# Performance work log

Measured on AMD Instinct MI355X. Metric: run time of the kernel, lower is better.

## Reference

```python
import jax, jax.numpy as jnp
import numpy as np

LN_EPS = 1e-5


def setup_inputs() -> dict:
    key = jax.random.key(0)
    ks = jax.random.split(key, 10)
    N, E, B = 20000, 320000, 16
    node_dim, cond_dim, out_dim = 256, 512, 256
    return {
        "node_feats": jax.random.normal(ks[0], (N, node_dim), dtype=jnp.float32),
        "cond_feats": jax.random.normal(ks[1], (B, cond_dim), dtype=jnp.float32),
        "batch_ids": jax.random.randint(ks[2], (N,), 0, B),
        "node_j_ids": jax.random.randint(ks[3], (E,), 0, N),
        "node_i_ids": jax.random.randint(ks[4], (E,), 0, N),
        "edge_w": jax.random.uniform(ks[5], (E, 1), dtype=jnp.float32),
        "edge_p": jax.random.uniform(ks[6], (E, 1), dtype=jnp.float32),
        "Wc": jax.random.normal(ks[7], (cond_dim, 2 * out_dim), dtype=jnp.float32) * (cond_dim ** -0.5),
        "bc": jax.random.normal(ks[8], (2 * out_dim,), dtype=jnp.float32) * 0.02,
        "Wl": jax.random.normal(ks[9], (node_dim, out_dim), dtype=jnp.float32) * (node_dim ** -0.5),
    }


def reference(node_feats, cond_feats, batch_ids, node_j_ids, node_i_ids,
              edge_w, edge_p, Wc, bc, Wl):
    N = node_feats.shape[0]
    # --- FiLM fusion ---
    gb = cond_feats @ Wc + bc                       # [B, 2*out_dim]
    gamma, beta = jnp.split(gb, 2, axis=-1)
    gamma = gamma + 1.0
    x = node_feats @ Wl                             # [N, out_dim]
    # non-affine LayerNorm over last dim
    mu = jnp.mean(x, axis=-1, keepdims=True)
    var = jnp.mean(jnp.square(x - mu), axis=-1, keepdims=True)
    x = (x - mu) * jax.lax.rsqrt(var + LN_EPS)
    x = x * gamma[batch_ids] + beta[batch_ids]      # per-node FiLM via batch gather
    x = jax.nn.relu(x)
    # --- message passing: gather -> weight -> scatter-add ---
    edge_weights = edge_w * edge_p                  # [E, 1]
    msg = x[node_j_ids] * edge_weights              # [E, out_dim]
    agg = jax.ops.segment_sum(msg, node_i_ids, num_segments=N)
    return jax.nn.relu(agg)
```

## Files before the change

### kernel.cpp

```cpp
#include <hip/hip_runtime.h>
#include <hip/hip_bf16.h>

#define OUT_DIM 256
#define COND_DIM 512
#define NODE_DIM 256
#define TM 32
#define LDA 264
#define LN_EPS 1e-5f
#define CAP 64
#define POISON 0xAAAAAAAAu
#define CHUNK 4096
#define EPT 16
#define NBINS 256
#define BCAP 2560

typedef __attribute__((ext_vector_type(8))) short bf16x8;
typedef __attribute__((ext_vector_type(8))) unsigned short u16x8;
typedef __attribute__((ext_vector_type(4))) float f32x4;

__device__ inline unsigned short f2bf(float f) {
    unsigned u = __float_as_uint(f);
    u += 0x7fffu + ((u >> 16) & 1u);
    return (unsigned short)(u >> 16);
}
__device__ inline float bf2f(unsigned short b) {
    return __uint_as_float((unsigned)b << 16);
}

__global__ __launch_bounds__(256) void f1_prep_kernel(
        const int* __restrict__ ni, const int* __restrict__ nj,
        const float* __restrict__ ew, const float* __restrict__ ep,
        unsigned* __restrict__ gcur, unsigned* __restrict__ coarse_ij,
        float* __restrict__ coarse_w, int E, int f1b,
        const float* __restrict__ Wl, unsigned short* __restrict__ WlT,
        const float* __restrict__ cond, const float* __restrict__ Wc,
        const float* __restrict__ bc, float* __restrict__ gamma, float* __restrict__ beta) {
    __shared__ float lds[64 * 65];
    __shared__ unsigned cnt[NBINS], base[NBINS];
    int t = threadIdx.x;

    if (blockIdx.x < (unsigned)f1b) {
        cnt[t] = 0;
        __syncthreads();
        unsigned ijr[EPT]; float wr[EPT]; unsigned rbr[EPT];
        int e0 = blockIdx.x * CHUNK;
        #pragma unroll
        for (int k = 0; k < EPT; ++k) {
            int e = e0 + k * 256 + t;
            if (e < E) {
                unsigned i = (unsigned)ni[e];
                unsigned j = (unsigned)nj[e];
                float w = ew[e] * ep[e];
                unsigned b = i >> 7;
                unsigned r = atomicAdd(&cnt[b], 1u);
                ijr[k] = (i << 16) | j;
                wr[k]  = w;
                rbr[k] = r | (b << 20);
            } else rbr[k] = 0xFFFFFFFFu;
        }
        __syncthreads();
        {
            unsigned c = cnt[t];
            base[t] = c ? (atomicAdd(&gcur[t], c) - POISON) : 0u;
        }
        __syncthreads();
        #pragma unroll
        for (int k = 0; k < EPT; ++k) {
            if (rbr[k] != 0xFFFFFFFFu) {
                unsigned b = rbr[k] >> 20;
                unsigned pos = base[b] + (rbr[k] & 0xFFFFFu);
                if (pos < BCAP) {
                    unsigned idx = b * BCAP + pos;
                    coarse_ij[idx] = ijr[k];
                    coarse_w[idx]  = wr[k];
                }
            }
        }
        return;
    }

    int pb = blockIdx.x - f1b;
    if (pb < 16) {
        float (*tile)[65] = (float(*)[65])lds;
        int bx = pb & 3, by = pb >> 2;
        int tr = t >> 6, tc = t & 63;
        #pragma unroll
        for (int rr = 0; rr < 64; rr += 4)
            tile[rr + tr][tc] = Wl[(by * 64 + rr + tr) * OUT_DIM + bx * 64 + tc];
        __syncthreads();
        #pragma unroll
        for (int rr = 0; rr < 64; rr += 4) {
            int n = bx * 64 + rr + tr;
            int k = by * 64 + tc;
            WlT[n * NODE_DIM + k] = f2bf(tile[tc][rr + tr]);
        }
    } else {
        int bf = pb - 16;
        int b = bf >> 1, half = bf & 1;
        int o = half * 256 + t;
        float* c = lds;
        for (int k = t; k < COND_DIM; k += 256) c[k] = cond[b * COND_DIM + k];
        __syncthreads();
        float acc = bc[o];
        for (int k = 0; k < COND_DIM; k += 4) {
            float4 cv = *(const float4*)&c[k];
            acc += cv.x * Wc[(k + 0) * 512 + o];
            acc += cv.y * Wc[(k + 1) * 512 + o];
            acc += cv.z * Wc[(k + 2) * 512 + o];
            acc += cv.w * Wc[(k + 3) * 512 + o];
        }
        if (half == 0) gamma[b * 256 + t] = acc + 1.0f;
        else           beta[b * 256 + t] = acc;
    }
}

__global__ __launch_bounds__(256) void f2_gemm_kernel(
        const unsigned* __restrict__ gcur, const unsigned* __restrict__ coarse_ij,
        const float* __restrict__ coarse_w, unsigned* __restrict__ epk,
        unsigned* __restrict__ cursor, int NB,
        const float* __restrict__ nf, const unsigned short* __restrict__ WlT,
        const int* __restrict__ batch_ids, const float* __restrict__ gamma,
        const float* __restrict__ beta, unsigned short* __restrict__ xout, int N) {
    __shared__ __align__(16) unsigned short Atile[TM * LDA];
    __shared__ float part_s[TM][2], part_s2[TM][2];
    __shared__ int bid_s[TM];
    __shared__ unsigned lcur[128];
    int t = threadIdx.x;

    if (blockIdx.x < (unsigned)NB) {
        int b = blockIdx.x;
        if (t < 128) lcur[t] = 0;
        __syncthreads();
        unsigned cntb = gcur[b] - POISON;
        if (cntb > BCAP) cntb = BCAP;
        for (unsigned r = t; r < cntb; r += 256) {
            unsigned ij = coarse_ij[(unsigned)b * BCAP + r];
            float w = coarse_w[(unsigned)b * BCAP + r];
            unsigned i = ij >> 16;
            unsigned c = atomicAdd(&lcur[i & 127u], 1u);
            if (c < CAP)
                epk[(i << 6) + c] = (ij & 0xFFFFu) | ((unsigned)f2bf(w) << 16);
        }
        __syncthreads();
        if (t < 128) cursor[(unsigned)b * 128 + t] = lcur[t];
        return;
    }

    int n0 = (blockIdx.x - NB) * TM;

    #pragma unroll
    for (int it = 0; it < 8; ++it) {
        int idx = t + it * 256;
        int r = idx >> 6;
        int c4 = idx & 63;
        int row = n0 + r;
        float4 v;
        if (row < N) v = *(const float4*)&nf[(size_t)row * NODE_DIM + c4 * 4];
        else         v = make_float4(0.f, 0.f, 0.f, 0.f);
        unsigned* dst = (unsigned*)&Atile[r * LDA + c4 * 4];
        dst[0] = (unsigned)f2bf(v.x) | ((unsigned)f2bf(v.y) << 16);
        dst[1] = (unsigned)f2bf(v.z) | ((unsigned)f2bf(v.w) << 16);
    }
    if (t < TM) bid_s[t] = (n0 + t < N) ? batch_ids[n0 + t] : 0;
    __syncthreads();

    int wave = t >> 6;
    int lane = t & 63;
    int l = lane & 15;
    int quad = lane >> 4;
    int rowbase = (wave & 1) * 16;
    int colbase = (wave >> 1) * 128;
    int half = wave >> 1;

    f32x4 acc[8];
    #pragma unroll
    for (int ct = 0; ct < 8; ++ct) acc[ct] = (f32x4){0.f, 0.f, 0.f, 0.f};

    const unsigned short* Abase = &Atile[(rowbase + l) * LDA + quad * 8];
    const unsigned short* Bbase = &WlT[(colbase + l) * NODE_DIM + quad * 8];

    #pragma unroll
    for (int ks = 0; ks < 8; ++ks) {
        bf16x8 a = *(const bf16x8*)(Abase + ks * 32);
        #pragma unroll
        for (int ct = 0; ct < 8; ++ct) {
            bf16x8 b = *(const bf16x8*)(Bbase + ct * 16 * NODE_DIM + ks * 32);
            acc[ct] = __builtin_amdgcn_mfma_f32_16x16x32_bf16(a, b, acc[ct], 0, 0, 0);
        }
    }

    #pragma unroll
    for (int reg = 0; reg < 4; ++reg) {
        float s = 0.f, s2 = 0.f;
        #pragma unroll
        for (int ct = 0; ct < 8; ++ct) {
            float v = acc[ct][reg];
            s += v; s2 += v * v;
        }
        #pragma unroll
        for (int off = 1; off <= 8; off <<= 1) {
            s += __shfl_xor(s, off);
            s2 += __shfl_xor(s2, off);
        }
        if (l == 0) {
            int r = rowbase + quad * 4 + reg;
            part_s[r][half] = s;
            part_s2[r][half] = s2;
        }
    }
    __syncthreads();

    #pragma unroll
    for (int reg = 0; reg < 4; ++reg) {
        int lrow = rowbase + quad * 4 + reg;
        float S = part_s[lrow][0] + part_s[lrow][1];
        float S2 = part_s2[lrow][0] + part_s2[lrow][1];
        float mu = S * (1.f / OUT_DIM);
        float var = S2 * (1.f / OUT_DIM) - mu * mu;
        float rs = rsqrtf(var + LN_EPS);
        int grow = n0 + lrow;
        int bid = bid_s[lrow];
        const float* gg = &gamma[bid * OUT_DIM];
        const float* gb = &beta[bid * OUT_DIM];
        if (grow < N) {
            unsigned short* orow = &xout[(size_t)grow * OUT_DIM];
            #pragma unroll
            for (int ct = 0; ct < 8; ++ct) {
                int col = colbase + ct * 16 + l;
                float v = (acc[ct][reg] - mu) * rs;
                v = v * gg[col] + gb[col];
                orow[col] = f2bf(fmaxf(v, 0.f));
            }
        }
    }
}

__global__ void agg_kernel(const unsigned short* __restrict__ x, const unsigned* __restrict__ epk,
                           const unsigned* __restrict__ cursor, float* __restrict__ out, int N) {
    int node = blockIdx.x * 4 + (threadIdx.x >> 6);
    int lane = threadIdx.x & 63;
    if (node >= N) return;
    int deg = (int)cursor[node];
    if (deg > CAP) deg = CAP;
    int s = node << 6;
    int e = s + deg;
    int half = lane >> 5;
    int li = lane & 31;

    float a[8];
    #pragma unroll
    for (int k = 0; k < 8; ++k) a[k] = 0.f;

    {
        unsigned pk[8];
        #pragma unroll
        for (int q = 0; q < 8; ++q) pk[q] = epk[s + 2 * q + half];
        float w[8];
        #pragma unroll
        for (int q = 0; q < 8; ++q)
            w[q] = (2 * q + half < deg) ? bf2f((unsigned short)(pk[q] >> 16)) : 0.f;
        u16x8 v[8];
        #pragma unroll
        for (int q = 0; q < 8; ++q)
            v[q] = *(const u16x8*)&x[(size_t)(pk[q] & 0xFFFFu) * OUT_DIM + li * 8];
        #pragma unroll
        for (int q = 0; q < 8; ++q) {
            #pragma unroll
            for (int k = 0; k < 8; ++k) a[k] += bf2f(v[q][k]) * w[q];
        }
    }

    for (int p = s + 16; p < e; p += 8) {
        int i0 = p + 0 + half, i1 = p + 2 + half, i2 = p + 4 + half, i3 = p + 6 + half;
        unsigned pk0 = epk[i0];
        unsigned pk1 = epk[i1];
        unsigned pk2 = epk[i2];
        unsigned pk3 = epk[i3];
        u16x8 v0 = *(const u16x8*)&x[(size_t)(pk0 & 0xFFFFu) * OUT_DIM + li * 8];
        u16x8 v1 = *(const u16x8*)&x[(size_t)(pk1 & 0xFFFFu) * OUT_DIM + li * 8];
        u16x8 v2 = *(const u16x8*)&x[(size_t)(pk2 & 0xFFFFu) * OUT_DIM + li * 8];
        u16x8 v3 = *(const u16x8*)&x[(size_t)(pk3 & 0xFFFFu) * OUT_DIM + li * 8];
        float w0 = (i0 < e) ? bf2f((unsigned short)(pk0 >> 16)) : 0.f;
        float w1 = (i1 < e) ? bf2f((unsigned short)(pk1 >> 16)) : 0.f;
        float w2 = (i2 < e) ? bf2f((unsigned short)(pk2 >> 16)) : 0.f;
        float w3 = (i3 < e) ? bf2f((unsigned short)(pk3 >> 16)) : 0.f;
        #pragma unroll
        for (int k = 0; k < 8; ++k) {
            a[k] += bf2f(v0[k]) * w0;
            a[k] += bf2f(v1[k]) * w1;
            a[k] += bf2f(v2[k]) * w2;
            a[k] += bf2f(v3[k]) * w3;
        }
    }

    #pragma unroll
    for (int k = 0; k < 8; ++k) a[k] += __shfl_xor(a[k], 32);

    f32x4 o;
    int kb = half * 4;
    o[0] = fmaxf(a[kb + 0], 0.f);
    o[1] = fmaxf(a[kb + 1], 0.f);
    o[2] = fmaxf(a[kb + 2], 0.f);
    o[3] = fmaxf(a[kb + 3], 0.f);
    __builtin_nontemporal_store(o, (f32x4*)&out[(size_t)node * OUT_DIM + li * 8 + kb]);
}

extern "C" void kernel_launch(void* const* d_in, const int* in_sizes, int n_in,
                              void* d_out, int out_size, void* d_ws, size_t ws_size,
                              hipStream_t stream) {
    const float* node_feats = (const float*)d_in[0];
    const float* cond_feats = (const float*)d_in[1];
    const int*   batch_ids  = (const int*)d_in[2];
    const int*   node_j     = (const int*)d_in[3];
    const int*   node_i     = (const int*)d_in[4];
    const float* edge_w     = (const float*)d_in[5];
    const float* edge_p     = (const float*)d_in[6];
    const float* Wc         = (const float*)d_in[7];
    const float* bc         = (const float*)d_in[8];
    const float* Wl         = (const float*)d_in[9];
    float* out = (float*)d_out;

    const int N = in_sizes[2];
    const int E = in_sizes[3];
    const int B = in_sizes[1] / COND_DIM;

    const int NB = (N + 127) / 128;

    char* ws = (char*)d_ws;
    float* gamma     = (float*)ws;  ws += (size_t)B * OUT_DIM * 4;
    float* beta      = (float*)ws;  ws += (size_t)B * OUT_DIM * 4;
    unsigned short* x   = (unsigned short*)ws;  ws += (size_t)N * OUT_DIM * 2;
    unsigned short* WlT = (unsigned short*)ws;  ws += (size_t)NODE_DIM * OUT_DIM * 2;
    unsigned* cursor = (unsigned*)ws;  ws += (size_t)NB * 128 * 4;
    unsigned* epk    = (unsigned*)ws;  ws += (size_t)N * CAP * 4;
    unsigned* gcur   = (unsigned*)ws;  ws += (size_t)NBINS * 4;
    unsigned* coarse_ij = (unsigned*)ws;  ws += (size_t)NBINS * BCAP * 4;
    float*    coarse_w  = (float*)ws;     ws += (size_t)NBINS * BCAP * 4;

    int nblk = (N + TM - 1) / TM;
    int f1b = (E + CHUNK - 1) / CHUNK;

    f1_prep_kernel<<<f1b + 48, 256, 0, stream>>>(node_i, node_j, edge_w, edge_p,
                                                 gcur, coarse_ij, coarse_w, E, f1b,
                                                 Wl, WlT, cond_feats, Wc, bc, gamma, beta);
    f2_gemm_kernel<<<NB + nblk, 256, 0, stream>>>(gcur, coarse_ij, coarse_w, epk, cursor, NB,
                                                  node_feats, WlT, batch_ids,
                                                  gamma, beta, x, N);
    agg_kernel<<<(N + 3) / 4, 256, 0, stream>>>(x, epk, cursor, out, N);
}
```

Before: 153.2 us.

## Fuse three kernels into one cooperative persistent kernel with grid syncs

Merges the prep, bin/GEMM and aggregation kernels into a single cooperative kernel that loops over work units in a persistent grid, separating phases with grid.sync(). The goal is to remove the launch gaps and tail effects between three kernel launches. In exchange, grid-wide barriers cost something, occupancy is capped by the cooperative grid (at most 1024 blocks under launch_bounds(256,4)), and the phases that used to run as large grids now run as strided loops. Grid size is cached in a static variable after the first call.

Result: slower. 327.5 us (+113.7%).

```diff
diff --git a/kernel.cpp b/kernel.cpp
--- a/kernel.cpp
+++ b/kernel.cpp
@@ -1,5 +1,8 @@
 #include <hip/hip_runtime.h>
+#include <hip/hip_cooperative_groups.h>
 #include <hip/hip_bf16.h>
+
+namespace cg = cooperative_groups;
 
 #define OUT_DIM 256
 #define COND_DIM 512
@@ -27,282 +30,281 @@
     return __uint_as_float((unsigned)b << 16);
 }
 
-__global__ __launch_bounds__(256) void f1_prep_kernel(
+__global__ __launch_bounds__(256, 4) void fused_kernel(
         const int* __restrict__ ni, const int* __restrict__ nj,
         const float* __restrict__ ew, const float* __restrict__ ep,
-        unsigned* __restrict__ gcur, unsigned* __restrict__ coarse_ij,
-        float* __restrict__ coarse_w, int E, int f1b,
-        const float* __restrict__ Wl, unsigned short* __restrict__ WlT,
-        const float* __restrict__ cond, const float* __restrict__ Wc,
-        const float* __restrict__ bc, float* __restrict__ gamma, float* __restrict__ beta) {
-    __shared__ float lds[64 * 65];
-    __shared__ unsigned cnt[NBINS], base[NBINS];
+        const float* __restrict__ Wl, const float* __restrict__ cond,
+        const float* __restrict__ Wc, const float* __restrict__ bc,
+        const float* __restrict__ nf, const int* __restrict__ batch_ids,
+        unsigned short* __restrict__ WlT, float* __restrict__ gamma, float* __restrict__ beta,
+        unsigned* __restrict__ gcur, unsigned* __restrict__ coarse_ij, float* __restrict__ coarse_w,
+        unsigned* __restrict__ epk, unsigned* __restrict__ cursor,
+        unsigned short* __restrict__ x, float* __restrict__ out,
+        int E, int N, int f1b, int NB, int nblk) {
+    cg::grid_group grid = cg::this_grid();
     int t = threadIdx.x;
 
-    if (blockIdx.x < (unsigned)f1b) {
-        cnt[t] = 0;
-        __syncthreads();
-        unsigned ijr[EPT]; float wr[EPT]; unsigned rbr[EPT];
-        int e0 = blockIdx.x * CHUNK;
-        #pragma unroll
-        for (int k = 0; k < EPT; ++k) {
-            int e = e0 + k * 256 + t;
-            if (e < E) {
-                unsigned i = (unsigned)ni[e];
-                unsigned j = (unsigned)nj[e];
-                float w = ew[e] * ep[e];
-                unsigned b = i >> 7;
-                unsigned r = atomicAdd(&cnt[b], 1u);
-                ijr[k] = (i << 16) | j;
-                wr[k]  = w;
-                rbr[k] = r | (b << 20);
-            } else rbr[k] = 0xFFFFFFFFu;
-        }
-        __syncthreads();
-        {
-            unsigned c = cnt[t];
-            base[t] = c ? (atomicAdd(&gcur[t], c) - POISON) : 0u;
-        }
-        __syncthreads();
-        #pragma unroll
-        for (int k = 0; k < EPT; ++k) {
-            if (rbr[k] != 0xFFFFFFFFu) {
-                unsigned b = rbr[k] >> 20;
-                unsigned pos = base[b] + (rbr[k] & 0xFFFFFu);
-                if (pos < BCAP) {
-                    unsigned idx = b * BCAP + pos;
-                    coarse_ij[idx] = ijr[k];
-                    coarse_w[idx]  = wr[k];
-                }
-            }
-        }
-        return;
-    }
-
-    int pb = blockIdx.x - f1b;
-    if (pb < 16) {
-        float (*tile)[65] = (float(*)[65])lds;
-        int bx = pb & 3, by = pb >> 2;
-        int tr = t >> 6, tc = t & 63;
-        #pragma unroll
-        for (int rr = 0; rr < 64; rr += 4)
-            tile[rr + tr][tc] = Wl[(by * 64 + rr + tr) * OUT_DIM + bx * 64 + tc];
-        __syncthreads();
-        #pragma unroll
-        for (int rr = 0; rr < 64; rr += 4) {
-            int n = bx * 64 + rr + tr;
-            int k = by * 64 + tc;
-            WlT[n * NODE_DIM + k] = f2bf(tile[tc][rr + tr]);
-        }
-    } else {
-        int bf = pb - 16;
-        int b = bf >> 1, half = bf & 1;
-        int o = half * 256 + t;
-        float* c = lds;
-        for (int k = t; k < COND_DIM; k += 256) c[k] = cond[b * COND_DIM + k];
-        __syncthreads();
-        float acc = bc[o];
-        for (int k = 0; k < COND_DIM; k += 4) {
-            float4 cv = *(const float4*)&c[k];
-            acc += cv.x * Wc[(k + 0) * 512 + o];
-            acc += cv.y * Wc[(k + 1) * 512 + o];
-            acc += cv.z * Wc[(k + 2) * 512 + o];
-            acc += cv.w * Wc[(k + 3) * 512 + o];
-        }
-        if (half == 0) gamma[b * 256 + t] = acc + 1.0f;
-        else           beta[b * 256 + t] = acc;
-    }
-}
-
-__global__ __launch_bounds__(256) void f2_gemm_kernel(
-        const unsigned* __restrict__ gcur, const unsigned* __restrict__ coarse_ij,
-        const float* __restrict__ coarse_w, unsigned* __restrict__ epk,
-        unsigned* __restrict__ cursor, int NB,
-        const float* __restrict__ nf, const unsigned short* __restrict__ WlT,
-        const int* __restrict__ batch_ids, const float* __restrict__ gamma,
-        const float* __restrict__ beta, unsigned short* __restrict__ xout, int N) {
     __shared__ __align__(16) unsigned short Atile[TM * LDA];
     __shared__ float part_s[TM][2], part_s2[TM][2];
     __shared__ int bid_s[TM];
     __shared__ unsigned lcur[128];
-    int t = threadIdx.x;
-
-    if (blockIdx.x < (unsigned)NB) {
-        int b = blockIdx.x;
-        if (t < 128) lcur[t] = 0;
+    __shared__ unsigned cnt[NBINS], base[NBINS];
+
+    for (int u = blockIdx.x; u < f1b + 48; u += gridDim.x) {
         __syncthreads();
-        unsigned cntb = gcur[b] - POISON;
-        if (cntb > BCAP) cntb = BCAP;
-        for (unsigned r = t; r < cntb; r += 256) {
-            unsigned ij = coarse_ij[(unsigned)b * BCAP + r];
-            float w = coarse_w[(unsigned)b * BCAP + r];
-            unsigned i = ij >> 16;
-            unsigned c = atomicAdd(&lcur[i & 127u], 1u);
-            if (c < CAP)
-                epk[(i << 6) + c] = (ij & 0xFFFFu) | ((unsigned)f2bf(w) << 16);
-        }
-        __syncthreads();
-        if (t < 128) cursor[(unsigned)b * 128 + t] = lcur[t];
-        return;
-    }
-
-    int n0 = (blockIdx.x - NB) * TM;
-
-    #pragma unroll
-    for (int it = 0; it < 8; ++it) {
-        int idx = t + it * 256;
-        int r = idx >> 6;
-        int c4 = idx & 63;
-        int row = n0 + r;
-        float4 v;
-        if (row < N) v = *(const float4*)&nf[(size_t)row * NODE_DIM + c4 * 4];
-        else         v = make_float4(0.f, 0.f, 0.f, 0.f);
-        unsigned* dst = (unsigned*)&Atile[r * LDA + c4 * 4];
-        dst[0] = (unsigned)f2bf(v.x) | ((unsigned)f2bf(v.y) << 16);
-        dst[1] = (unsigned)f2bf(v.z) | ((unsigned)f2bf(v.w) << 16);
-    }
-    if (t < TM) bid_s[t] = (n0 + t < N) ? batch_ids[n0 + t] : 0;
-    __syncthreads();
-
-    int wave = t >> 6;
-    int lane = t & 63;
-    int l = lane & 15;
-    int quad = lane >> 4;
-    int rowbase = (wave & 1) * 16;
-    int colbase = (wave >> 1) * 128;
-    int half = wave >> 1;
-
-    f32x4 acc[8];
-    #pragma unroll
-    for (int ct = 0; ct < 8; ++ct) acc[ct] = (f32x4){0.f, 0.f, 0.f, 0.f};
-
-    const unsigned short* Abase = &Atile[(rowbase + l) * LDA + quad * 8];
-    const unsigned short* Bbase = &WlT[(colbase + l) * NODE_DIM + quad * 8];
-
-    #pragma unroll
-    for (int ks = 0; ks < 8; ++ks) {
-        bf16x8 a = *(const bf16x8*)(Abase + ks * 32);
-        #pragma unroll
-        for (int ct = 0; ct < 8; ++ct) {
-            bf16x8 b = *(const bf16x8*)(Bbase + ct * 16 * NODE_DIM + ks * 32);
-            acc[ct] = __builtin_amdgcn_mfma_f32_16x16x32_bf16(a, b, acc[ct], 0, 0, 0);
+        if (u < f1b) {
+            cnt[t] = 0;
+            __syncthreads();
+            unsigned ijr[EPT]; float wr[EPT]; unsigned rbr[EPT];
+            int e0 = u * CHUNK;
+            #pragma unroll
+            for (int k = 0; k < EPT; ++k) {
+                int e = e0 + k * 256 + t;
+                if (e < E) {
+                    unsigned i = (unsigned)ni[e];
+                    unsigned j = (unsigned)nj[e];
+                    float w = ew[e] * ep[e];
+                    unsigned b = i >> 7;
+                    unsigned r = atomicAdd(&cnt[b], 1u);
+                    ijr[k] = (i << 16) | j;
+                    wr[k]  = w;
+                    rbr[k] = r | (b << 20);
+                } else rbr[k] = 0xFFFFFFFFu;
+            }
+            __syncthreads();
+            {
+                unsigned c = cnt[t];
+                base[t] = c ? (atomicAdd(&gcur[t], c) - POISON) : 0u;
+            }
+            __syncthreads();
+            #pragma unroll
+            for (int k = 0; k < EPT; ++k) {
+                if (rbr[k] != 0xFFFFFFFFu) {
+                    unsigned b = rbr[k] >> 20;
+                    unsigned pos = base[b] + (rbr[k] & 0xFFFFFu);
+                    if (pos < BCAP) {
+                        unsigned idx = b * BCAP + pos;
+                        coarse_ij[idx] = ijr[k];
+                        coarse_w[idx]  = wr[k];
+                    }
+                }
+            }
+        } else {
+            int pb = u - f1b;
+            if (pb < 16) {
+                float (*tile)[65] = (float(*)[65])Atile;
+                int bx = pb & 3, by = pb >> 2;
+                int tr = t >> 6, tc = t & 63;
+                #pragma unroll
+                for (int rr = 0; rr < 64; rr += 4)
+                    tile[rr + tr][tc] = Wl[(by * 64 + rr + tr) * OUT_DIM + bx * 64 + tc];
+                __syncthreads();
+                #pragma unroll
+                for (int rr = 0; rr < 64; rr += 4) {
+                    int n = bx * 64 + rr + tr;
+                    int k = by * 64 + tc;
+                    WlT[n * NODE_DIM + k] = f2bf(tile[tc][rr + tr]);
+                }
+            } else {
+                int bf = pb - 16;
+                int b = bf >> 1, half = bf & 1;
+                int o = half * 256 + t;
+                float* c = (float*)Atile;
+                for (int k = t; k < COND_DIM; k += 256) c[k] = cond[b * COND_DIM + k];
+                __syncthreads();
+                float acc = bc[o];
+                for (int k = 0; k < COND_DIM; k += 4) {
+                    float4 cv = *(const float4*)&c[k];
+                    acc += cv.x * Wc[(k + 0) * 512 + o];
+                    acc += cv.y * Wc[(k + 1) * 512 + o];
+                    acc += cv.z * Wc[(k + 2) * 512 + o];
+                    acc += cv.w * Wc[(k + 3) * 512 + o];
+                }
+                if (half == 0) gamma[b * 256 + t] = acc + 1.0f;
+                else           beta[b * 256 + t] = acc;
+            }
         }
     }
-
-    #pragma unroll
-    for (int reg = 0; reg < 4; ++reg) {
-        float s = 0.f, s2 = 0.f;
-        #pragma unroll
-        for (int ct = 0; ct < 8; ++ct) {
-            float v = acc[ct][reg];
-            s += v; s2 += v * v;
-        }
-        #pragma unroll
-        for (int off = 1; off <= 8; off <<= 1) {
-            s += __shfl_xor(s, off);
-            s2 += __shfl_xor(s2, off);
-        }
-        if (l == 0) {
-            int r = rowbase + quad * 4 + reg;
-            part_s[r][half] = s;
-            part_s2[r][half] = s2;
+    grid.sync();
+
+    for (int u = blockIdx.x; u < NB + nblk; u += gridDim.x) {
+        __syncthreads();
+        if (u < NB) {
+            int b = u;
+            if (t < 128) lcur[t] = 0;
+            __syncthreads();
+            unsigned cntb = gcur[b] - POISON;
+            if (cntb > BCAP) cntb = BCAP;
+            for (unsigned r = t; r < cntb; r += 256) {
+                unsigned ij = coarse_ij[(unsigned)b * BCAP + r];
+                float w = coarse_w[(unsigned)b * BCAP + r];
+                unsigned i = ij >> 16;
+                unsigned c = atomicAdd(&lcur[i & 127u], 1u);
+                if (c < CAP)
+                    epk[(i << 6) + c] = (ij & 0xFFFFu) | ((unsigned)f2bf(w) << 16);
+            }
+            __syncthreads();
+            if (t < 128) cursor[(unsigned)b * 128 + t] = lcur[t];
+        } else {
+            int n0 = (u - NB) * TM;
+            #pragma unroll
+            for (int it = 0; it < 8; ++it) {
+                int idx = t + it * 256;
+                int r = idx >> 6;
+                int c4 = idx & 63;
+                int row = n0 + r;
+                float4 v;
+                if (row < N) v = *(const float4*)&nf[(size_t)row * NODE_DIM + c4 * 4];
+                else         v = make_float4(0.f, 0.f, 0.f, 0.f);
+                unsigned* dst = (unsigned*)&Atile[r * LDA + c4 * 4];
+                dst[0] = (unsigned)f2bf(v.x) | ((unsigned)f2bf(v.y) << 16);
+                dst[1] = (unsigned)f2bf(v.z) | ((unsigned)f2bf(v.w) << 16);
+            }
+            if (t < TM) bid_s[t] = (n0 + t < N) ? batch_ids[n0 + t] : 0;
+            __syncthreads();
+
+            int wave = t >> 6;
+            int lane = t & 63;
+            int l = lane & 15;
+            int quad = lane >> 4;
+            int rowbase = (wave & 1) * 16;
+            int colbase = (wave >> 1) * 128;
+            int half = wave >> 1;
+
+            f32x4 acc[8];
+            #pragma unroll
+            for (int ct = 0; ct < 8; ++ct) acc[ct] = (f32x4){0.f, 0.f, 0.f, 0.f};
+
+            const unsigned short* Abase = &Atile[(rowbase + l) * LDA + quad * 8];
+            const unsigned short* Bbase = &WlT[(colbase + l) * NODE_DIM + quad * 8];
+
+            #pragma unroll
+            for (int ks = 0; ks < 8; ++ks) {
+                bf16x8 a = *(const bf16x8*)(Abase + ks * 32);
+                #pragma unroll
+                for (int ct = 0; ct < 8; ++ct) {
+                    bf16x8 b = *(const bf16x8*)(Bbase + ct * 16 * NODE_DIM + ks * 32);
+                    acc[ct] = __builtin_amdgcn_mfma_f32_16x16x32_bf16(a, b, acc[ct], 0, 0, 0);
+                }
+            }
+
+            #pragma unroll
+            for (int reg = 0; reg < 4; ++reg) {
+                float s = 0.f, s2 = 0.f;
+                #pragma unroll
+                for (int ct = 0; ct < 8; ++ct) {
+                    float v = acc[ct][reg];
+                    s += v; s2 += v * v;
+                }
+                #pragma unroll
+                for (int off = 1; off <= 8; off <<= 1) {
+                    s += __shfl_xor(s, off);
+                    s2 += __shfl_xor(s2, off);
+                }
+                if (l == 0) {
+                    int r = rowbase + quad * 4 + reg;
+                    part_s[r][half] = s;
+                    part_s2[r][half] = s2;
+                }
+            }
+            __syncthreads();
+
+            #pragma unroll
+            for (int reg = 0; reg < 4; ++reg) {
+                int lrow = rowbase + quad * 4 + reg;
+                float S = part_s[lrow][0] + part_s[lrow][1];
+                float S2 = part_s2[lrow][0] + part_s2[lrow][1];
+                float mu = S * (1.f / OUT_DIM);
+                float var = S2 * (1.f / OUT_DIM) - mu * mu;
+                float rs = rsqrtf(var + LN_EPS);
+                int grow = n0 + lrow;
+                int bid = bid_s[lrow];
+                const float* gg = &gamma[bid * OUT_DIM];
+                const float* gb = &beta[bid * OUT_DIM];
+                if (grow < N) {
+                    unsigned short* orow = &x[(size_t)grow * OUT_DIM];
+                    #pragma unroll
+                    for (int ct = 0; ct < 8; ++ct) {
+                        int col = colbase + ct * 16 + l;
+                        float v = (acc[ct][reg] - mu) * rs;
+                        v = v * gg[col] + gb[col];
+                        orow[col] = f2bf(fmaxf(v, 0.f));
+                    }
+                }
+            }
         }
     }
-    __syncthreads();
-
-    #pragma unroll
-    for (int reg = 0; reg < 4; ++reg) {
-        int lrow = rowbase + quad * 4 + reg;
-        float S = part_s[lrow][0] + part_s[lrow][1];
-        float S2 = part_s2[lrow][0] + part_s2[lrow][1];
-        float mu = S * (1.f / OUT_DIM);
-        float var = S2 * (1.f / OUT_DIM) - mu * mu;
-        float rs = rsqrtf(var + LN_EPS);
-        int grow = n0 + lrow;
-        int bid = bid_s[lrow];
-        const float* gg = &gamma[bid * OUT_DIM];
-        const float* gb = &beta[bid * OUT_DIM];
-        if (grow < N) {
-            unsigned short* orow = &xout[(size_t)grow * OUT_DIM];
-            #pragma unroll
-            for (int ct = 0; ct < 8; ++ct) {
-                int col = colbase + ct * 16 + l;
-                float v = (acc[ct][reg] - mu) * rs;
-                v = v * gg[col] + gb[col];
-                orow[col] = f2bf(fmaxf(v, 0.f));
+    grid.sync();
+
+    int ngroups = (N + 3) >> 2;
+    for (int g = blockIdx.x; g < ngroups; g += gridDim.x) {
+        int node = g * 4 + (t >> 6);
+        if (node >= N) continue;
+        int lane = t & 63;
+        int deg = (int)cursor[node];
+        if (deg > CAP) deg = CAP;
+        int s = node << 6;
+        int e = s + deg;
+        int half = lane >> 5;
+        int li = lane & 31;
+
+        float a[8];
+        #pragma unroll
+        for (int k = 0; k < 8; ++k) a[k] = 0.f;
+
+        {
+            unsigned pk[8];
+            #pragma unroll
+            for (int q = 0; q < 8; ++q) pk[q] = epk[s + 2 * q + half];
+            float w[8];
+            #pragma unroll
+            for (int q = 0; q < 8; ++q)
+                w[q] = (2 * q + half < deg) ? bf2f((unsigned short)(pk[q] >> 16)) : 0.f;
+            u16x8 v[8];
+            #pragma unroll
+            for (int q = 0; q < 8; ++q)
+                v[q] = *(const u16x8*)&x[(size_t)(pk[q] & 0xFFFFu) * OUT_DIM + li * 8];
+            #pragma unroll
+            for (int q = 0; q < 8; ++q) {
+                #pragma unroll
+                for (int k = 0; k < 8; ++k) a[k] += bf2f(v[q][k]) * w[q];
             }
         }
+
+        for (int p = s + 16; p < e; p += 8) {
+            int i0 = p + 0 + half, i1 = p + 2 + half, i2 = p + 4 + half, i3 = p + 6 + half;
+            unsigned pk0 = epk[i0];
+            unsigned pk1 = epk[i1];
+            unsigned pk2 = epk[i2];
+            unsigned pk3 = epk[i3];
+            u16x8 v0 = *(const u16x8*)&x[(size_t)(pk0 & 0xFFFFu) * OUT_DIM + li * 8];
+            u16x8 v1 = *(const u16x8*)&x[(size_t)(pk1 & 0xFFFFu) * OUT_DIM + li * 8];
+            u16x8 v2 = *(const u16x8*)&x[(size_t)(pk2 & 0xFFFFu) * OUT_DIM + li * 8];
+            u16x8 v3 = *(const u16x8*)&x[(size_t)(pk3 & 0xFFFFu) * OUT_DIM + li * 8];
+            float w0 = (i0 < e) ? bf2f((unsigned short)(pk0 >> 16)) : 0.f;
+            float w1 = (i1 < e) ? bf2f((unsigned short)(pk1 >> 16)) : 0.f;
+            float w2 = (i2 < e) ? bf2f((unsigned short)(pk2 >> 16)) : 0.f;
+            float w3 = (i3 < e) ? bf2f((unsigned short)(pk3 >> 16)) : 0.f;
+            #pragma unroll
+            for (int k = 0; k < 8; ++k) {
+                a[k] += bf2f(v0[k]) * w0;
+                a[k] += bf2f(v1[k]) * w1;
+                a[k] += bf2f(v2[k]) * w2;
+                a[k] += bf2f(v3[k]) * w3;
+            }
+        }
+
+        #pragma unroll
+        for (int k = 0; k < 8; ++k) a[k] += __shfl_xor(a[k], 32);
+
+        f32x4 o;
+        int kb = half * 4;
+        o[0] = fmaxf(a[kb + 0], 0.f);
+        o[1] = fmaxf(a[kb + 1], 0.f);
+        o[2] = fmaxf(a[kb + 2], 0.f);
+        o[3] = fmaxf(a[kb + 3], 0.f);
+        __builtin_nontemporal_store(o, (f32x4*)&out[(size_t)node * OUT_DIM + li * 8 + kb]);
     }
-}
-
-__global__ void agg_kernel(const unsigned short* __restrict__ x, const unsigned* __restrict__ epk,
-                           const unsigned* __restrict__ cursor, float* __restrict__ out, int N) {
-    int node = blockIdx.x * 4 + (threadIdx.x >> 6);
-    int lane = threadIdx.x & 63;
-    if (node >= N) return;
-    int deg = (int)cursor[node];
-    if (deg > CAP) deg = CAP;
-    int s = node << 6;
-    int e = s + deg;
-    int half = lane >> 5;
-    int li = lane & 31;
-
-    float a[8];
-    #pragma unroll
-    for (int k = 0; k < 8; ++k) a[k] = 0.f;
-
-    {
-        unsigned pk[8];
-        #pragma unroll
-        for (int q = 0; q < 8; ++q) pk[q] = epk[s + 2 * q + half];
-        float w[8];
-        #pragma unroll
-        for (int q = 0; q < 8; ++q)
-            w[q] = (2 * q + half < deg) ? bf2f((unsigned short)(pk[q] >> 16)) : 0.f;
-        u16x8 v[8];
-        #pragma unroll
-        for (int q = 0; q < 8; ++q)
-            v[q] = *(const u16x8*)&x[(size_t)(pk[q] & 0xFFFFu) * OUT_DIM + li * 8];
-        #pragma unroll
-        for (int q = 0; q < 8; ++q) {
-            #pragma unroll
-            for (int k = 0; k < 8; ++k) a[k] += bf2f(v[q][k]) * w[q];
-        }
-    }
-
-    for (int p = s + 16; p < e; p += 8) {
-        int i0 = p + 0 + half, i1 = p + 2 + half, i2 = p + 4 + half, i3 = p + 6 + half;
-        unsigned pk0 = epk[i0];
-        unsigned pk1 = epk[i1];
-        unsigned pk2 = epk[i2];
-        unsigned pk3 = epk[i3];
-        u16x8 v0 = *(const u16x8*)&x[(size_t)(pk0 & 0xFFFFu) * OUT_DIM + li * 8];
-        u16x8 v1 = *(const u16x8*)&x[(size_t)(pk1 & 0xFFFFu) * OUT_DIM + li * 8];
-        u16x8 v2 = *(const u16x8*)&x[(size_t)(pk2 & 0xFFFFu) * OUT_DIM + li * 8];
-        u16x8 v3 = *(const u16x8*)&x[(size_t)(pk3 & 0xFFFFu) * OUT_DIM + li * 8];
-        float w0 = (i0 < e) ? bf2f((unsigned short)(pk0 >> 16)) : 0.f;
-        float w1 = (i1 < e) ? bf2f((unsigned short)(pk1 >> 16)) : 0.f;
-        float w2 = (i2 < e) ? bf2f((unsigned short)(pk2 >> 16)) : 0.f;
-        float w3 = (i3 < e) ? bf2f((unsigned short)(pk3 >> 16)) : 0.f;
-        #pragma unroll
-        for (int k = 0; k < 8; ++k) {
-            a[k] += bf2f(v0[k]) * w0;
-            a[k] += bf2f(v1[k]) * w1;
-            a[k] += bf2f(v2[k]) * w2;
-            a[k] += bf2f(v3[k]) * w3;
-        }
-    }
-
-    #pragma unroll
-    for (int k = 0; k < 8; ++k) a[k] += __shfl_xor(a[k], 32);
-
-    f32x4 o;
-    int kb = half * 4;
-    o[0] = fmaxf(a[kb + 0], 0.f);
-    o[1] = fmaxf(a[kb + 1], 0.f);
-    o[2] = fmaxf(a[kb + 2], 0.f);
-    o[3] = fmaxf(a[kb + 3], 0.f);
-    __builtin_nontemporal_store(o, (f32x4*)&out[(size_t)node * OUT_DIM + li * 8 + kb]);
 }
 
 extern "C" void kernel_launch(void* const* d_in, const int* in_sizes, int n_in,
@@ -320,11 +322,10 @@
     const float* Wl         = (const float*)d_in[9];
     float* out = (float*)d_out;
 
-    const int N = in_sizes[2];
-    const int E = in_sizes[3];
+    int E = in_sizes[3];
+    int N = in_sizes[2];
     const int B = in_sizes[1] / COND_DIM;
-
-    const int NB = (N + 127) / 128;
+    int NB = (N + 127) / 128;
 
     char* ws = (char*)d_ws;
     float* gamma     = (float*)ws;  ws += (size_t)B * OUT_DIM * 4;
@@ -340,11 +341,25 @@
     int nblk = (N + TM - 1) / TM;
     int f1b = (E + CHUNK - 1) / CHUNK;
 
-    f1_prep_kernel<<<f1b + 48, 256, 0, stream>>>(node_i, node_j, edge_w, edge_p,
-                                                 gcur, coarse_ij, coarse_w, E, f1b,
-                                                 Wl, WlT, cond_feats, Wc, bc, gamma, beta);
-    f2_gemm_kernel<<<NB + nblk, 256, 0, stream>>>(gcur, coarse_ij, coarse_w, epk, cursor, NB,
-                                                  node_feats, WlT, batch_ids,
-                                                  gamma, beta, x, N);
-    agg_kernel<<<(N + 3) / 4, 256, 0, stream>>>(x, epk, cursor, out, N);
+    static int coopGrid = 0;
+    if (coopGrid == 0) {
+        int maxb = 0;
+        hipOccupancyMaxActiveBlocksPerMultiprocessor(&maxb, fused_kernel, 256, 0);
+        if (maxb < 1) maxb = 1;
+        long g = (long)maxb * 256;
+        if (g > 1024) g = 1024;
+        coopGrid = (int)g;
+    }
+
+    void* args[] = {
+        (void*)&node_i, (void*)&node_j, (void*)&edge_w, (void*)&edge_p,
+        (void*)&Wl, (void*)&cond_feats, (void*)&Wc, (void*)&bc,
+        (void*)&node_feats, (void*)&batch_ids,
+        (void*)&WlT, (void*)&gamma, (void*)&beta,
+        (void*)&gcur, (void*)&coarse_ij, (void*)&coarse_w,
+        (void*)&epk, (void*)&cursor, (void*)&x, (void*)&out,
+        (void*)&E, (void*)&N, (void*)&f1b, (void*)&NB, (void*)&nblk
+    };
+    hipLaunchCooperativeKernel((void*)fused_kernel, dim3(coopGrid), dim3(256),
+                               args, 0, stream);
 }
```
